# Performance work log

Measured on AMD Instinct MI355X. Metric: run time of the kernel, lower is better.

The kernel has to match this reference:

```python
import jax, jax.numpy as jnp
import numpy as np

# ST-GCN spatial graph convolution:
#   f = Conv2d_1x1(x)                       -> [N, K*C_out, T, V]
#   f = reshape to [N, K, C_out, T, V]
#   out[n,c,t,w] = sum_{k,v} f[n,k,c,t,v] * A[k,v,w]

N, C_IN, T, V = 32, 64, 300, 25
K, C_OUT = 3, 64


def setup_inputs() -> dict:
    key = jax.random.key(0)
    k1, k2, k3, k4 = jax.random.split(key, 4)
    x = jax.random.normal(k1, (N, C_IN, T, V), dtype=jnp.float32)
    W = jax.random.normal(k2, (K * C_OUT, C_IN), dtype=jnp.float32) * 0.05  # 1x1 conv weight
    b = jax.random.normal(k3, (K * C_OUT,), dtype=jnp.float32) * 0.05
    # Normalized adjacency stack [K, V, V] (row-normalized random graph, stands in
    # for adj.normalize(create_adjacency_matrices(strat)))
    A = jax.random.uniform(k4, (K, V, V), dtype=jnp.float32)
    A = A / jnp.sum(A, axis=-1, keepdims=True)
    return {"x": x, "W": W, "b": b, "A": A}


def reference(x, W, b, A):
    # 1x1 conv == per-(t,v) channel projection
    f = jnp.einsum("nctv,oc->notv", x, W) + b[None, :, None, None]  # [N, K*C_out, T, V]
    f = f.reshape(N, K, C_OUT, T, V)
    # adjacency-weighted neighbor aggregation
    out = jnp.einsum("nkctv,kvw->nctw", f, A)  # [N, C_out, T, V]
    return out
```

## Files before the change

kernel.cpp:

```cpp
#include <hip/hip_runtime.h>
#include <hip/hip_bf16.h>


#define CIN   64
#define T_    300
#define V_    25
#define COUT  64
#define NITEM 9600
#define NWAVE 4096

#define WS_W2 0
#define WS_AH 24576
#define WS_BO 49152
#define WS_BYTES 57344

#define LDS_W2 0
#define LDS_AH 24576
#define LDS_BO 49152
#define SMEM_BYTES 57344

typedef short  bf16x8 __attribute__((ext_vector_type(8)));
typedef float  f32x4  __attribute__((ext_vector_type(4)));

__device__ __forceinline__ unsigned short cvt_bf16(float f) {
    union { __hip_bfloat16 h; unsigned short u; } cv;
    cv.h = __float2bfloat16(f);
    return cv.u;
}
__device__ __forceinline__ unsigned pk2(float a, float b) {
    return (unsigned)cvt_bf16(a) | ((unsigned)cvt_bf16(b) << 16);
}
union fragu { bf16x8 v; unsigned u[4]; };

#define GLL16(g, s) __builtin_amdgcn_global_load_lds( \
    (const __attribute__((address_space(1))) void*)(g), \
    (__attribute__((address_space(3))) void*)(s), 16, 0, 0)

__global__ void gcn_prep(const float* __restrict__ W, const float* __restrict__ bias,
                         const float* __restrict__ A, unsigned char* __restrict__ ws)
{
    const int tid = blockIdx.x * 256 + threadIdx.x;
    for (int i = tid; i < 4 * 6 * 64 * 8; i += 4096) {
        const int e = i & 7, lane = (i >> 3) & 63, ck = i >> 9;
        const int kap = ck % 6, ct = ck / 6;
        const int lr = lane & 15, lq = lane >> 4;
        const int row = (kap >> 1) * COUT + ct * 16 + lr;
        const int col = 32 * (kap & 1) + 16 * (e >> 2) + 4 * lq + (e & 3);
        reinterpret_cast<unsigned short*>(ws + WS_W2)[i] = cvt_bf16(W[row * CIN + col]);
    }
    for (int i = tid; i < 4 * 96 * 32; i += 4096) {
        const int vp = i & 31, kw = (i >> 5) % 96, dd = (i >> 5) / 96;
        const int k = kw >> 5, w = kw & 31, v = vp - dd;
        const float val = (v >= 0 && v < V_ && w < V_) ? A[(k * V_ + v) * V_ + w] : 0.f;
        reinterpret_cast<unsigned short*>(ws + WS_AH)[i] = cvt_bf16(val);
    }
    for (int i = tid; i < 32 * 64; i += 4096) {
        const int w = i >> 6, c = i & 63;
        float s = 0.f;
        if (w < V_) {
            for (int k = 0; k < 3; ++k) {
                float sa = 0.f;
                for (int v = 0; v < V_; ++v) sa += A[(k * V_ + v) * V_ + w];
                s += bias[k * COUT + c] * sa;
            }
        }
        reinterpret_cast<float*>(ws + WS_BO)[i] = s;
    }
}

__global__ __launch_bounds__(512, 4) void gcn_main(
    const float* __restrict__ x, const unsigned char* __restrict__ ws,
    float* __restrict__ out)
{
    __shared__ __align__(16) unsigned char smem[SMEM_BYTES];

    const int tid = threadIdx.x;
    const int wv = tid >> 6, l = tid & 63, lr = l & 15, lq = l >> 4;
    const int wid = blockIdx.x * 8 + wv;

    auto loadx = [&](int it, f32x4 (&xa)[4], f32x4 (&xg)[4]) {
        const int n = it / T_, t = it % T_, d = t & 3;
        const float* xrow = x + (size_t)(n * CIN + lr) * (T_ * V_) + (t * V_ - d) + 8 * lq;
        #pragma unroll
        for (int mi = 0; mi < 4; ++mi) {
            const float* p = xrow + (size_t)mi * 16 * (T_ * V_);
            xa[mi] = *reinterpret_cast<const f32x4*>(p);
            xg[mi] = *reinterpret_cast<const f32x4*>(p + (lq < 3 ? 4 : 0));
        }
    };
    auto cvtx = [&](f32x4 (&xa)[4], f32x4 (&xg)[4], bf16x8 (&xf)[4]) {
        #pragma unroll
        for (int mi = 0; mi < 4; ++mi) {
            fragu f;
            f.u[0] = pk2(xa[mi][0], xa[mi][1]);
            f.u[1] = pk2(xa[mi][2], xa[mi][3]);
            f.u[2] = pk2(xg[mi][0], xg[mi][1]);
            f.u[3] = pk2(xg[mi][2], xg[mi][3]);
            xf[mi] = f.v;
        }
    };
    auto process = [&](int it, bf16x8 (&xf)[4]) {
        const int n = it / T_, t = it % T_, d = t & 3;
        f32x4 oacc[4][2];
        #pragma unroll
        for (int ct = 0; ct < 4; ++ct)
            #pragma unroll
            for (int nt = 0; nt < 2; ++nt)
                oacc[ct][nt] = *reinterpret_cast<const f32x4*>(
                    smem + LDS_BO + ((ct * 2 + nt) << 10) + l * 16);
        #pragma unroll
        for (int k = 0; k < 3; ++k) {
            bf16x8 ahf[2];
            #pragma unroll
            for (int j = 0; j < 2; ++j)
                ahf[j] = *reinterpret_cast<const bf16x8*>(
                    smem + LDS_AH + ((d * 6 + 2 * k + j) << 10) + l * 16);
            f32x4 y[4][2];
            #pragma unroll
            for (int mi = 0; mi < 4; ++mi)
                #pragma unroll
                for (int j = 0; j < 2; ++j)
                    y[mi][j] = (f32x4){0.f, 0.f, 0.f, 0.f};
            #pragma unroll
            for (int j = 0; j < 2; ++j)
                #pragma unroll
                for (int mi = 0; mi < 4; ++mi)
                    y[mi][j] = __builtin_amdgcn_mfma_f32_16x16x32_bf16(
                        xf[mi], ahf[j], y[mi][j], 0, 0, 0);
            #pragma unroll
            for (int kl = 0; kl < 2; ++kl) {
                bf16x8 w2f[4];
                #pragma unroll
                for (int ct = 0; ct < 4; ++ct)
                    w2f[ct] = *reinterpret_cast<const bf16x8*>(
                        smem + LDS_W2 + ((ct * 6 + 2 * k + kl) << 10) + l * 16);
                #pragma unroll
                for (int nt = 0; nt < 2; ++nt) {
                    fragu bb;
                    bb.u[0] = pk2(y[2 * kl][nt][0],     y[2 * kl][nt][1]);
                    bb.u[1] = pk2(y[2 * kl][nt][2],     y[2 * kl][nt][3]);
                    bb.u[2] = pk2(y[2 * kl + 1][nt][0], y[2 * kl + 1][nt][1]);
                    bb.u[3] = pk2(y[2 * kl + 1][nt][2], y[2 * kl + 1][nt][3]);
                    #pragma unroll
                    for (int ct = 0; ct < 4; ++ct)
                        oacc[ct][nt] = __builtin_amdgcn_mfma_f32_16x16x32_bf16(
                            w2f[ct], bb.v, oacc[ct][nt], 0, 0, 0);
                }
            }
        }
        float* ob = out + ((size_t)(n * COUT) * T_ + t) * V_;
        #pragma unroll
        for (int ct = 0; ct < 4; ++ct) {
            #pragma unroll
            for (int r = 0; r < 4; ++r) {
                const int c = 16 * ct + 4 * lq + r;
                float* op = ob + (size_t)c * (T_ * V_);
                op[lr] = oacc[ct][0][r];
                if (lr < 9) op[16 + lr] = oacc[ct][1][r];
            }
        }
    };

    f32x4 xa0[4], xg0[4], xa1[4], xg1[4];
    loadx(wid, xa0, xg0);

    for (int s = wv; s < 56; s += 8) {
        const unsigned char* src;
        if (s < 24) {
            src = ws + WS_W2 + s * 1024 + l * 16;
        } else if (s < 48) {
            src = ws + WS_AH + (s - 24) * 1024 + 64 * lr + 16 * lq;
        } else {
            const int i2 = s - 48, nt = i2 & 1, ct = i2 >> 1;
            src = ws + WS_BO + (16 * nt + lr) * 256 + 64 * ct + 16 * lq;
        }
        GLL16(src, smem + s * 1024);
    }
    __builtin_amdgcn_sched_barrier(0);
    __syncthreads();

    loadx(wid + NWAVE, xa1, xg1);
    __builtin_amdgcn_sched_barrier(0);

    bf16x8 xf[4];
    cvtx(xa0, xg0, xf);
    const bool has2 = wid + 2 * NWAVE < NITEM;
    if (has2) loadx(wid + 2 * NWAVE, xa0, xg0);
    __builtin_amdgcn_sched_barrier(0);
    process(wid, xf);

    cvtx(xa1, xg1, xf);
    process(wid + NWAVE, xf);

    if (has2) {
        cvtx(xa0, xg0, xf);
        process(wid + 2 * NWAVE, xf);
    }
}

extern "C" void kernel_launch(void* const* d_in, const int* in_sizes, int n_in,
                              void* d_out, int out_size, void* d_ws, size_t ws_size,
                              hipStream_t stream) {
    const float* x    = (const float*)d_in[0];
    const float* W    = (const float*)d_in[1];
    const float* bias = (const float*)d_in[2];
    const float* A    = (const float*)d_in[3];
    float* out = (float*)d_out;
    unsigned char* ws = (unsigned char*)d_ws;

    hipLaunchKernelGGL(gcn_prep, dim3(16), dim3(256), 0, stream, W, bias, A, ws);
    hipLaunchKernelGGL(gcn_main, dim3(512), dim3(512), 0, stream, x, ws, out);
}
```

Baseline: 45.83 us.

## Assign contiguous work items per wave and single-buffer x prefetch

Work items are now assigned to each wave as a contiguous run: the first 1408 waves take 3 consecutive items and the rest take 2, replacing the strided wid + k*NWAVE assignment. The x prefetch drops from two register buffers to one, with the next item's load issued right after converting the current one. The first conversion and second load are moved ahead of the LDS-staging barrier so they overlap the workspace copy. This aims to cut register pressure and improve locality of adjacent time steps, at the cost of less prefetch depth.

```diff
diff --git a/kernel.cpp b/kernel.cpp
--- a/kernel.cpp
+++ b/kernel.cpp
@@ -6,8 +6,6 @@
 #define T_    300
 #define V_    25
 #define COUT  64
-#define NITEM 9600
-#define NWAVE 4096
 
 #define WS_W2 0
 #define WS_AH 24576
@@ -77,6 +75,8 @@
     const int tid = threadIdx.x;
     const int wv = tid >> 6, l = tid & 63, lr = l & 15, lq = l >> 4;
     const int wid = blockIdx.x * 8 + wv;
+    const bool g3 = wid < 1408;
+    const int it0 = g3 ? 3 * wid : 2 * wid + 1408;
 
     auto loadx = [&](int it, f32x4 (&xa)[4], f32x4 (&xg)[4]) {
         const int n = it / T_, t = it % T_, d = t & 3;
@@ -88,7 +88,7 @@
             xg[mi] = *reinterpret_cast<const f32x4*>(p + (lq < 3 ? 4 : 0));
         }
     };
-    auto cvtx = [&](f32x4 (&xa)[4], f32x4 (&xg)[4], bf16x8 (&xf)[4]) {
+    auto cvtx = [&](const f32x4 (&xa)[4], const f32x4 (&xg)[4], bf16x8 (&xf)[4]) {
         #pragma unroll
         for (int mi = 0; mi < 4; ++mi) {
             fragu f;
@@ -99,7 +99,7 @@
             xf[mi] = f.v;
         }
     };
-    auto process = [&](int it, bf16x8 (&xf)[4]) {
+    auto run = [&](int it, const bf16x8 (&xf)[4]) {
         const int n = it / T_, t = it % T_, d = t & 3;
         f32x4 oacc[4][2];
         #pragma unroll
@@ -161,8 +161,8 @@
         }
     };
 
-    f32x4 xa0[4], xg0[4], xa1[4], xg1[4];
-    loadx(wid, xa0, xg0);
+    f32x4 xa[4], xg[4];
+    loadx(it0, xa, xg);
 
     for (int s = wv; s < 56; s += 8) {
         const unsigned char* src;
@@ -177,24 +177,24 @@
         GLL16(src, smem + s * 1024);
     }
     __builtin_amdgcn_sched_barrier(0);
+
+    bf16x8 xf[4];
+    cvtx(xa, xg, xf);
+    loadx(it0 + 1, xa, xg);
+    __builtin_amdgcn_sched_barrier(0);
+
     __syncthreads();
 
-    loadx(wid + NWAVE, xa1, xg1);
+    run(it0, xf);
+
+    cvtx(xa, xg, xf);
+    if (g3) loadx(it0 + 2, xa, xg);
     __builtin_amdgcn_sched_barrier(0);
-
-    bf16x8 xf[4];
-    cvtx(xa0, xg0, xf);
-    const bool has2 = wid + 2 * NWAVE < NITEM;
-    if (has2) loadx(wid + 2 * NWAVE, xa0, xg0);
-    __builtin_amdgcn_sched_barrier(0);
-    process(wid, xf);
-
-    cvtx(xa1, xg1, xf);
-    process(wid + NWAVE, xf);
-
-    if (has2) {
-        cvtx(xa0, xg0, xf);
-        process(wid + 2 * NWAVE, xf);
+    run(it0 + 1, xf);
+
+    if (g3) {
+        cvtx(xa, xg, xf);
+        run(it0 + 2, xf);
     }
 }
 
```

Measured after the change: 49.55 us. 8.1% more time.
